# Performance work log

Hardware: AMD Instinct MI355X
Metric: run time of the kernel (lower is better)

## Reference

```python
import jax, jax.numpy as jnp
import numpy as np

D_MODEL = 512
H = 8
D_HEAD = D_MODEL // H  # 64


def setup_inputs() -> dict:
    key = jax.random.key(0)
    ks = jax.random.split(key, 11)
    b, n = 4, 2048
    s_in = 1.0 / np.sqrt(D_MODEL)
    inp = {
        "q": jax.random.normal(ks[0], (b, n, D_MODEL), jnp.float32),
        "k": jax.random.normal(ks[1], (b, n, D_MODEL), jnp.float32),
        "v": jax.random.normal(ks[2], (b, n, D_MODEL), jnp.float32),
        # torch Linear weights stored here as (in, out) so x @ W + b
        "Wq": jax.random.normal(ks[3], (D_MODEL, D_HEAD), jnp.float32) * s_in,
        "bq": jnp.zeros((D_HEAD,), jnp.float32),
        "Wk": jax.random.normal(ks[4], (D_MODEL, D_HEAD), jnp.float32) * s_in,
        "bk": jnp.zeros((D_HEAD,), jnp.float32),
        "Wv": jax.random.normal(ks[5], (D_MODEL, D_HEAD), jnp.float32) * s_in,
        "bv": jnp.zeros((D_HEAD,), jnp.float32),
        "Wo": jax.random.normal(ks[6], (D_MODEL, D_MODEL), jnp.float32) * s_in,
        "bo": jnp.zeros((D_MODEL,), jnp.float32),
    }
    return inp


def reference(q, k, v, Wq, bq, Wk, bk, Wv, bv, Wo, bo):
    # Original repeats q/k/v across H=8 heads and applies the SAME Linear
    # (d_model -> d_head) to every head, so all heads are identical.
    # We compute the projection once and tile the concatenated output,
    # which is mathematically identical to the torch code.
    qp = q @ Wq + bq  # (b, n, d_head)
    kp = k @ Wk + bk
    vp = v @ Wv + bv
    scale = 1.0 / jnp.sqrt(jnp.asarray(D_HEAD, qp.dtype))
    scores = jnp.einsum("bnd,bmd->bnm", qp, kp) * scale  # (b, n, n) full score matrix
    attn = jax.nn.softmax(scores, axis=-1)
    o = jnp.einsum("bnm,bmd->bnd", attn, vp)  # (b, n, d_head)
    out = jnp.tile(o, (1, 1, H))  # concat of H identical heads -> (b, n, d_model)
    return out @ Wo + bo
```

## Files before the change

### kernel.cpp

```cpp
#include <hip/hip_runtime.h>

typedef float f32x4 __attribute__((ext_vector_type(4)));
typedef short bf16x8 __attribute__((ext_vector_type(8)));
typedef __bf16 bf16x2_t __attribute__((ext_vector_type(2)));
typedef unsigned int u32;
typedef unsigned long long u64;

__device__ __forceinline__ u32 pk2(float a, float b){
  bf16x2_t h; h[0] = (__bf16)a; h[1] = (__bf16)b;
  return __builtin_bit_cast(u32, h);
}
__device__ __forceinline__ unsigned short f2bf(float f){
  __bf16 h = (__bf16)f;
  return __builtin_bit_cast(unsigned short, h);
}
__device__ __forceinline__ float bf2f(unsigned short h){
  u32 u = ((u32)h) << 16;
  return __builtin_bit_cast(float, u);
}

#define WS_WOF   98304u
#define WS_QF    131072u
#define WS_KF    655360u
#define WS_VF    1179648u

#define QSCALE 0.18033688011112042f

__device__ __forceinline__ bf16x8 wfrag(const float* __restrict__ W, int kc, int cg,
                                        int g, int ln){
  const float* p = W + (size_t)(kc*32 + g*8)*64 + cg*16 + ln;
  union { bf16x8 v8; u32 w[4]; } u;
  #pragma unroll
  for (int j = 0; j < 4; ++j)
    u.w[j] = pk2(p[(2*j)*64], p[(2*j+1)*64]);
  return u.v8;
}

__global__ __launch_bounds__(128) void k_proj(const float* __restrict__ q,
    const float* __restrict__ kmat, const float* __restrict__ v,
    const float* __restrict__ bq, const float* __restrict__ bk,
    const float* __restrict__ bv, const float* __restrict__ Wq,
    const float* __restrict__ Wk, const float* __restrict__ Wv,
    const float* __restrict__ Wo, unsigned short* __restrict__ wsu){
  const int which = blockIdx.y;
  const int t = threadIdx.x;
  if (which == 3){
    int id = blockIdx.x*128 + t;
    int j = id & 7, lf = (id >> 3) & 63, kt = (id >> 9) & 1, c16 = id >> 10;
    int n = c16*16 + (lf & 15), k = kt*32 + (lf >> 4)*8 + j;
    float s = 0.f;
    #pragma unroll
    for (int h = 0; h < 8; ++h) s += Wo[(h*64 + k)*512 + n];
    wsu[WS_WOF + id] = f2bf(s);
    return;
  }

  __shared__ unsigned short Xs[2][2048];
  const float* X    = which==0 ? q  : (which==1 ? kmat : v);
  const float* bias = which==0 ? bq : (which==1 ? bk   : bv);
  const float* W    = which==0 ? Wq : (which==1 ? Wk   : Wv);
  const int rowbase = blockIdx.x * 32;
  const int w = t >> 6, l = t & 63, g = l >> 4, ln = l & 15;

  f32x4 acc[2][2];
  #pragma unroll
  for (int rt = 0; rt < 2; ++rt)
    #pragma unroll
    for (int ntl = 0; ntl < 2; ++ntl) acc[rt][ntl] = (f32x4){0.f,0.f,0.f,0.f};
  float bcol[2];
  #pragma unroll
  for (int ntl = 0; ntl < 2; ++ntl) bcol[ntl] = bias[(w*2+ntl)*16 + ln];

  f32x4 xr[4];
  bf16x8 bc[2][2], bn[2][2];

  #pragma unroll
  for (int j = 0; j < 4; ++j){
    int c = t + j*128; int row = c >> 4, kc = c & 15;
    xr[j] = __builtin_nontemporal_load(reinterpret_cast<const f32x4*>(X + (rowbase+row)*512 + kc*4));
  }
  #pragma unroll
  for (int ntl = 0; ntl < 2; ++ntl)
    #pragma unroll
    for (int kt = 0; kt < 2; ++kt)
      bc[ntl][kt] = wfrag(W, 0*2+kt, w*2+ntl, g, ln);

  #pragma unroll
  for (int i = 0; i < 8; ++i){
    char* Xc = reinterpret_cast<char*>(Xs[i & 1]);
    #pragma unroll
    for (int j = 0; j < 4; ++j){
      int c = t + j*128; int row = c >> 4, kc = c & 15;
      u64 pk = (u64)pk2(xr[j][0], xr[j][1]) | ((u64)pk2(xr[j][2], xr[j][3]) << 32);
      *reinterpret_cast<u64*>(Xc + row*128 + ((kc*8) ^ ((row&7)<<4))) = pk;
    }
    if (i < 7){
      #pragma unroll
      for (int j = 0; j < 4; ++j){
        int c = t + j*128; int row = c >> 4, kc = c & 15;
        xr[j] = __builtin_nontemporal_load(reinterpret_cast<const f32x4*>(X + (rowbase+row)*512 + (i+1)*64 + kc*4));
      }
    }
    __syncthreads();
    if (i < 7){
      #pragma unroll
      for (int ntl = 0; ntl < 2; ++ntl)
        #pragma unroll
        for (int kt = 0; kt < 2; ++kt)
          bn[ntl][kt] = wfrag(W, (i+1)*2+kt, w*2+ntl, g, ln);
    }
    bf16x8 a[2][2];
    #pragma unroll
    for (int rt = 0; rt < 2; ++rt){
      int arow = rt*16 + ln;
      #pragma unroll
      for (int kt = 0; kt < 2; ++kt)
        a[rt][kt] = *reinterpret_cast<const bf16x8*>(Xc + arow*128 + ((kt*64 + g*16) ^ ((arow&7)<<4)));
    }
    #pragma unroll
    for (int ntl = 0; ntl < 2; ++ntl)
      #pragma unroll
      for (int kt = 0; kt < 2; ++kt)
        #pragma unroll
        for (int rt = 0; rt < 2; ++rt)
          acc[rt][ntl] = __builtin_amdgcn_mfma_f32_16x16x32_bf16(a[rt][kt], bc[ntl][kt], acc[rt][ntl], 0, 0, 0);
    if (i < 7){
      #pragma unroll
      for (int ntl = 0; ntl < 2; ++ntl)
        #pragma unroll
        for (int kt = 0; kt < 2; ++kt)
          bc[ntl][kt] = bn[ntl][kt];
    }
  }

  char* Xb = reinterpret_cast<char*>(Xs[0]);
  __syncthreads();
  if (which < 2){
    const float sc = (which==0) ? QSCALE : 1.0f;
    #pragma unroll
    for (int rt = 0; rt < 2; ++rt)
      #pragma unroll
      for (int ntl = 0; ntl < 2; ++ntl)
        #pragma unroll
        for (int r = 0; r < 4; ++r){
          int row = rt*16 + g*4 + r, col = (w*2+ntl)*16 + ln;
          *reinterpret_cast<unsigned short*>(Xb + row*128 + ((col*2) ^ ((row&7)<<4))) =
              f2bf((acc[rt][ntl][r] + bcol[ntl]) * sc);
        }
    __syncthreads();
    unsigned short* base = (which==0)
        ? wsu + WS_QF + (unsigned)(((rowbase>>4) + w)*2)*512u
        : wsu + WS_KF + (unsigned)(rowbase>>11)*131072u + (unsigned)((((rowbase&2047)>>4) + w)*2)*512u;
    const int arow = w*16 + ln;
    #pragma unroll
    for (int kt = 0; kt < 2; ++kt){
      bf16x8 f = *reinterpret_cast<const bf16x8*>(Xb + arow*128 + ((kt*64 + g*16) ^ ((arow&7)<<4)));
      *reinterpret_cast<bf16x8*>(base + kt*512 + l*8) = f;
    }
  } else {
    #pragma unroll
    for (int rt = 0; rt < 2; ++rt)
      #pragma unroll
      for (int ntl = 0; ntl < 2; ++ntl)
        #pragma unroll
        for (int r = 0; r < 4; ++r){
          int kv = rt*16 + g*4 + r, d = (w*2+ntl)*16 + ln;
          *reinterpret_cast<unsigned short*>(Xb + d*64 + ((kv*2) ^ ((d&3)<<4))) =
              f2bf(acc[rt][ntl][r] + bcol[ntl]);
        }
    __syncthreads();
    unsigned short* vfb = wsu + WS_VF + (unsigned)(rowbase>>11)*131072u;
    const int kv32 = (rowbase & 2047) >> 5;
    #pragma unroll
    for (int dtl = 0; dtl < 2; ++dtl){
      int dt = w*2 + dtl;
      int rd = dt*16 + ln;
      bf16x8 f = *reinterpret_cast<const bf16x8*>(Xb + rd*64 + ((g*16) ^ ((rd&3)<<4)));
      *reinterpret_cast<bf16x8*>(vfb + (unsigned)((kv32*4 + dt)*64 + l)*8u) = f;
    }
  }
}

#define PSTR 72

__global__ __launch_bounds__(512) void k_attn(const unsigned short* __restrict__ wsu,
    const float* __restrict__ bo, float* __restrict__ out){
  __shared__ __attribute__((aligned(16))) unsigned char smem[42496];

  const int t = threadIdx.x;
  const int w = t >> 6, l = t & 63, g = l >> 4, ln = l & 15;
  const int bid = blockIdx.x;
  const int batch = (bid & 7) >> 1;
  const int tile  = ((bid & 1) << 5) | (bid >> 3);
  const int qbase = batch*2048 + tile*32;

  const unsigned short* qf  = wsu + WS_QF;
  const unsigned short* kfb = wsu + WS_KF + (unsigned)batch*131072u;
  const unsigned short* vfb = wsu + WS_VF + (unsigned)batch*131072u;
  const unsigned short* wof = wsu + WS_WOF;

  unsigned short* Pw  = (unsigned short*)(smem + w*4608);
  float*          pls = (float*)(smem + 36864);
  unsigned short* ob  = (unsigned short*)(smem + 37888);

  const int q16 = qbase >> 4;
  bf16x8 qa[2][2];
  #pragma unroll
  for (int rt = 0; rt < 2; ++rt)
    #pragma unroll
    for (int kt = 0; kt < 2; ++kt)
      qa[rt][kt] = *reinterpret_cast<const bf16x8*>(qf + (unsigned)(((q16+rt)*2 + kt)*64 + l)*8u);

  f32x4 o[4][2];
  #pragma unroll
  for (int dt = 0; dt < 4; ++dt)
    #pragma unroll
    for (int rt = 0; rt < 2; ++rt) o[dt][rt] = (f32x4){0.f,0.f,0.f,0.f};
  float ls[2] = {0.f, 0.f};

  const int kv0 = w * 256;

  #pragma unroll
  for (int it = 0; it < 4; ++it){
    const int kvb = kv0 + it*64;
    const int kv16 = kvb >> 4, kv32 = kvb >> 5;
    bf16x8 ka[4][2];
    #pragma unroll
    for (int ct = 0; ct < 4; ++ct)
      #pragma unroll
      for (int kt = 0; kt < 2; ++kt)
        ka[ct][kt] = *reinterpret_cast<const bf16x8*>(kfb + (unsigned)(((kv16+ct)*2 + kt)*64 + l)*8u);
    f32x4 st[4][2];
    #pragma unroll
    for (int ct = 0; ct < 4; ++ct)
      #pragma unroll
      for (int rt = 0; rt < 2; ++rt){
        st[ct][rt] = (f32x4){0.f,0.f,0.f,0.f};
        #pragma unroll
        for (int kt = 0; kt < 2; ++kt)
          st[ct][rt] = __builtin_amdgcn_mfma_f32_16x16x32_bf16(ka[ct][kt], qa[rt][kt], st[ct][rt], 0,0,0);
      }
    bf16x8 vb[4][2];
    #pragma unroll
    for (int dt = 0; dt < 4; ++dt)
      #pragma unroll
      for (int kvt = 0; kvt < 2; ++kvt)
        vb[dt][kvt] = *reinterpret_cast<const bf16x8*>(vfb + (unsigned)(((kv32+kvt)*4 + dt)*64 + l)*8u);

    #pragma unroll
    for (int rt = 0; rt < 2; ++rt){
      float p[4][4];
      float rs = 0.f;
      #pragma unroll
      for (int ct = 0; ct < 4; ++ct)
        #pragma unroll
        for (int r = 0; r < 4; ++r){
          p[ct][r] = exp2f(st[ct][rt][r]);
          rs += p[ct][r];
        }
      rs += __shfl_xor(rs, 16, 64);
      rs += __shfl_xor(rs, 32, 64);
      ls[rt] += rs;
      unsigned short* pr = Pw + (rt*16 + ln)*PSTR;
      #pragma unroll
      for (int ct = 0; ct < 4; ++ct){
        *reinterpret_cast<u32*>(pr + ct*16 + g*4)     = pk2(p[ct][0], p[ct][1]);
        *reinterpret_cast<u32*>(pr + ct*16 + g*4 + 2) = pk2(p[ct][2], p[ct][3]);
      }
    }
    bf16x8 pb[2][2];
    #pragma unroll
    for (int rt = 0; rt < 2; ++rt)
      #pragma unroll
      for (int kvt = 0; kvt < 2; ++kvt)
        pb[rt][kvt] = *reinterpret_cast<const bf16x8*>(Pw + (rt*16 + ln)*PSTR + kvt*32 + g*8);
    #pragma unroll
    for (int dt = 0; dt < 4; ++dt)
      #pragma unroll
      for (int rt = 0; rt < 2; ++rt)
        #pragma unroll
        for (int kvt = 0; kvt < 2; ++kvt)
          o[dt][rt] = __builtin_amdgcn_mfma_f32_16x16x32_bf16(vb[dt][kvt], pb[rt][kvt], o[dt][rt], 0,0,0);
  }

  if (l < 16){ pls[w*32 + ln] = ls[0]; pls[w*32 + 16 + ln] = ls[1]; }
  unsigned short* pow_ = (unsigned short*)(smem + w*4608);
  #pragma unroll
  for (int dt = 0; dt < 4; ++dt)
    #pragma unroll
    for (int rt = 0; rt < 2; ++rt){
      u32* dst = reinterpret_cast<u32*>(pow_ + (rt*16 + ln)*68 + dt*16 + g*4);
      dst[0] = pk2(o[dt][rt][0], o[dt][rt][1]);
      dst[1] = pk2(o[dt][rt][2], o[dt][rt][3]);
    }
  __syncthreads();

  #pragma unroll
  for (int i = 0; i < 4; ++i){
    int idx = t + i*512;
    int row = idx >> 6, d = idx & 63;
    float den = 0.f, num = 0.f;
    #pragma unroll
    for (int w2 = 0; w2 < 8; ++w2){
      den += pls[w2*32 + row];
      num += bf2f(*((const unsigned short*)(smem + w2*4608) + row*68 + d));
    }
    ob[row*PSTR + d] = f2bf(num / den);
  }
  __syncthreads();

  const int colbase = w*64;
  bf16x8 ao[2][2];
  #pragma unroll
  for (int rt = 0; rt < 2; ++rt)
    #pragma unroll
    for (int kt = 0; kt < 2; ++kt)
      ao[rt][kt] = *reinterpret_cast<const bf16x8*>(ob + (rt*16 + ln)*PSTR + kt*32 + g*8);
  f32x4 oc[2][4];
  #pragma unroll
  for (int rt = 0; rt < 2; ++rt)
    #pragma unroll
    for (int nt = 0; nt < 4; ++nt) oc[rt][nt] = (f32x4){0.f,0.f,0.f,0.f};
  #pragma unroll
  for (int nt = 0; nt < 4; ++nt){
    #pragma unroll
    for (int kt = 0; kt < 2; ++kt){
      bf16x8 b = *reinterpret_cast<const bf16x8*>(wof + (unsigned)(((w*4+nt)*2 + kt)*64 + l)*8u);
      #pragma unroll
      for (int rt = 0; rt < 2; ++rt)
        oc[rt][nt] = __builtin_amdgcn_mfma_f32_16x16x32_bf16(ao[rt][kt], b, oc[rt][nt], 0,0,0);
    }
  }
  #pragma unroll
  for (int nt = 0; nt < 4; ++nt){
    float bc = bo[colbase + nt*16 + ln];
    #pragma unroll
    for (int rt = 0; rt < 2; ++rt){
      #pragma unroll
      for (int r = 0; r < 4; ++r){
        int row = qbase + rt*16 + g*4 + r;
        __builtin_nontemporal_store(oc[rt][nt][r] + bc, &out[row*512 + colbase + nt*16 + ln]);
      }
    }
  }
}

extern "C" void kernel_launch(void* const* d_in, const int* in_sizes, int n_in,
                              void* d_out, int out_size, void* d_ws, size_t ws_size,
                              hipStream_t stream){
  const float* q  = (const float*)d_in[0];
  const float* k  = (const float*)d_in[1];
  const float* v  = (const float*)d_in[2];
  const float* Wq = (const float*)d_in[3];
  const float* bq = (const float*)d_in[4];
  const float* Wk = (const float*)d_in[5];
  const float* bk = (const float*)d_in[6];
  const float* Wv = (const float*)d_in[7];
  const float* bv = (const float*)d_in[8];
  const float* Wo = (const float*)d_in[9];
  const float* bo = (const float*)d_in[10];
  float* out = (float*)d_out;
  unsigned short* wsu = (unsigned short*)d_ws;

  k_proj<<<dim3(256, 4), dim3(128), 0, stream>>>(q, k, v, bq, bk, bv, Wq, Wk, Wv, Wo, wsu);
  k_attn<<<dim3(256), dim3(512), 0, stream>>>(wsu, bo, out);
}
```

Measured before the change: 33.04 us.

## Split KV range across blocks and add separate merge kernel for output projection

```diff
diff --git a/kernel.cpp b/kernel.cpp
--- a/kernel.cpp
+++ b/kernel.cpp
@@ -23,8 +23,11 @@
 #define WS_QF    131072u
 #define WS_KF    655360u
 #define WS_VF    1179648u
+#define WS_PNUM  851968u
+#define WS_PDEN  1900544u
 
 #define QSCALE 0.18033688011112042f
+#define PSTR 72
 
 __device__ __forceinline__ bf16x8 wfrag(const float* __restrict__ W, int kc, int cg,
                                         int g, int ln){
@@ -181,27 +184,27 @@
   }
 }
 
-#define PSTR 72
-
-__global__ __launch_bounds__(512) void k_attn(const unsigned short* __restrict__ wsu,
-    const float* __restrict__ bo, float* __restrict__ out){
-  __shared__ __attribute__((aligned(16))) unsigned char smem[42496];
+__global__ __launch_bounds__(512) void k_attn(unsigned short* __restrict__ wsu){
+  __shared__ __attribute__((aligned(16))) unsigned char smem[37888];
 
   const int t = threadIdx.x;
   const int w = t >> 6, l = t & 63, g = l >> 4, ln = l & 15;
   const int bid = blockIdx.x;
-  const int batch = (bid & 7) >> 1;
-  const int tile  = ((bid & 1) << 5) | (bid >> 3);
-  const int qbase = batch*2048 + tile*32;
+  const int xcd = bid & 7;
+  const int batch = xcd >> 1;
+  const int kvhalf = xcd & 1;
+  const int qtile = bid >> 3;
+  const int qg = w >> 2, kvs = w & 3;
+  const int qbase = batch*2048 + qtile*64 + qg*32;
+  const int kv0 = kvhalf*1024 + kvs*256;
 
   const unsigned short* qf  = wsu + WS_QF;
   const unsigned short* kfb = wsu + WS_KF + (unsigned)batch*131072u;
   const unsigned short* vfb = wsu + WS_VF + (unsigned)batch*131072u;
-  const unsigned short* wof = wsu + WS_WOF;
+  float* wsf = (float*)wsu;
 
   unsigned short* Pw  = (unsigned short*)(smem + w*4608);
   float*          pls = (float*)(smem + 36864);
-  unsigned short* ob  = (unsigned short*)(smem + 37888);
 
   const int q16 = qbase >> 4;
   bf16x8 qa[2][2];
@@ -217,8 +220,6 @@
     #pragma unroll
     for (int rt = 0; rt < 2; ++rt) o[dt][rt] = (f32x4){0.f,0.f,0.f,0.f};
   float ls[2] = {0.f, 0.f};
-
-  const int kv0 = w * 256;
 
   #pragma unroll
   for (int it = 0; it < 4; ++it){
@@ -295,17 +296,46 @@
     }
   __syncthreads();
 
-  #pragma unroll
-  for (int i = 0; i < 4; ++i){
+  const unsigned pb0 = (unsigned)(batch*64 + qtile*2);
+  #pragma unroll
+  for (int i = 0; i < 8; ++i){
     int idx = t + i*512;
-    int row = idx >> 6, d = idx & 63;
-    float den = 0.f, num = 0.f;
-    #pragma unroll
-    for (int w2 = 0; w2 < 8; ++w2){
-      den += pls[w2*32 + row];
-      num += bf2f(*((const unsigned short*)(smem + w2*4608) + row*68 + d));
-    }
-    ob[row*PSTR + d] = f2bf(num / den);
+    int qg2 = idx >> 11, row = (idx >> 6) & 31, d = idx & 63;
+    float num = 0.f;
+    #pragma unroll
+    for (int j = 0; j < 4; ++j)
+      num += bf2f(*((const unsigned short*)(smem + (qg2*4 + j)*4608) + row*68 + d));
+    wsf[WS_PNUM + (unsigned)(((pb0 + qg2)*2 + kvhalf))*2048u + row*64 + d] = num;
+    if (d == 0){
+      float den = 0.f;
+      #pragma unroll
+      for (int j = 0; j < 4; ++j) den += pls[(qg2*4 + j)*32 + row];
+      wsf[WS_PDEN + (unsigned)(((pb0 + qg2)*2 + kvhalf))*32u + row] = den;
+    }
+  }
+}
+
+__global__ __launch_bounds__(512) void k_merge(const unsigned short* __restrict__ wsu,
+    const float* __restrict__ bo, float* __restrict__ out){
+  __shared__ __attribute__((aligned(16))) unsigned short ob[32*PSTR];
+
+  const int t = threadIdx.x;
+  const int w = t >> 6, l = t & 63, g = l >> 4, ln = l & 15;
+  const int q32 = blockIdx.x, batch = blockIdx.y;
+  const int qbase = batch*2048 + q32*32;
+  const float* wsf = (const float*)wsu;
+  const unsigned short* wof = wsu + WS_WOF;
+
+  {
+    const int row = t >> 4, ds = (t & 15)*4;
+    const unsigned pi = (unsigned)((batch*64 + q32)*2);
+    f32x4 n0 = *reinterpret_cast<const f32x4*>(&wsf[WS_PNUM + pi*2048u + row*64 + ds]);
+    f32x4 n1 = *reinterpret_cast<const f32x4*>(&wsf[WS_PNUM + (pi+1)*2048u + row*64 + ds]);
+    float den = wsf[WS_PDEN + pi*32u + row] + wsf[WS_PDEN + (pi+1)*32u + row];
+    float rin = 1.0f / den;
+    u32* dst = reinterpret_cast<u32*>(&ob[row*PSTR + ds]);
+    dst[0] = pk2((n0[0]+n1[0])*rin, (n0[1]+n1[1])*rin);
+    dst[1] = pk2((n0[2]+n1[2])*rin, (n0[3]+n1[3])*rin);
   }
   __syncthreads();
 
@@ -363,5 +393,6 @@
   unsigned short* wsu = (unsigned short*)d_ws;
 
   k_proj<<<dim3(256, 4), dim3(128), 0, stream>>>(q, k, v, bq, bk, bv, Wq, Wk, Wv, Wo, wsu);
-  k_attn<<<dim3(256), dim3(512), 0, stream>>>(wsu, bo, out);
-}
+  k_attn<<<dim3(256), dim3(512), 0, stream>>>(wsu);
+  k_merge<<<dim3(64, 4), dim3(512), 0, stream>>>(wsu, bo, out);
+}
```

Result: slower. 37.14 us (+12.4%).
